# Performance work log

Measured on AMD Instinct MI355X. Metric: run time of the kernel, lower is better.

## Reference

```python
import jax, jax.numpy as jnp
import numpy as np

B, T, D, U = 128, 2048, 256, 512
ALPHA = 0.001


def hard_sigmoid(x):
    return jnp.clip(0.2 * x + 0.5, 0.0, 1.0)


def setup_inputs() -> dict:
    key = jax.random.key(0)
    k1, k2, k3 = jax.random.split(key, 3)
    x = jax.random.normal(k1, (B, T, D), dtype=jnp.float32)
    h0 = jnp.zeros((B, U), dtype=jnp.float32)
    c0 = jnp.zeros((B, U), dtype=jnp.float32)
    t0 = jnp.zeros((B, U), dtype=jnp.float32)
    # glorot-ish kernels
    kernel = jax.random.normal(k2, (D, 4 * U), dtype=jnp.float32) * (1.0 / np.sqrt(D))
    recurrent_kernel = jax.random.normal(k3, (U, 4 * U), dtype=jnp.float32) * (1.0 / np.sqrt(U))
    # bias zeros with forget-gate slice = 1 (unit_forget_bias)
    bias = jnp.zeros((4 * U,), dtype=jnp.float32).at[U:2 * U].set(1.0)
    # timegate: rows = period ~ U(10,100), shift ~ U(0,1000), r_on = 0.05
    rng = np.random.RandomState(0)
    timegate_kernel = jnp.asarray(
        np.vstack((rng.uniform(10, 100, U), rng.uniform(0, 1000, U), np.zeros(U) + 0.05)),
        dtype=jnp.float32)
    return {"x": x, "h0": h0, "c0": c0, "t0": t0, "kernel": kernel,
            "recurrent_kernel": recurrent_kernel, "bias": bias,
            "timegate_kernel": timegate_kernel}


def reference(x, h0, c0, t0, kernel, recurrent_kernel, bias, timegate_kernel):
    period = timegate_kernel[0]  # [U]
    shift = timegate_kernel[1]   # [U]
    r_on = timegate_kernel[2]    # [U]

    def step(carry, x_t):
        h, c, t = carry
        t = t + 1.0
        # fused gate pre-activations: [B, 4U]
        z = x_t @ kernel + h @ recurrent_kernel + bias
        zi, zf, zc, zo = jnp.split(z, 4, axis=-1)
        i = hard_sigmoid(zi)
        f = hard_sigmoid(zf)
        c_hat = f * c + i * jnp.tanh(zc)
        o = hard_sigmoid(zo)
        h_hat = o * jnp.tanh(c_hat)
        # phased time gate
        phi = (t - shift - period * jnp.floor((t - shift) / period)) / period
        k = jnp.where(phi <= r_on * 0.5, 2.0 * phi / r_on,
                      jnp.where(phi <= r_on, 2.0 - 2.0 * phi / r_on, ALPHA * phi))
        c_new = k * c_hat + (1.0 - k) * c
        h_new = k * h_hat + (1.0 - k) * h
        return (h_new, c_new, t), h_new

    xs = jnp.swapaxes(x, 0, 1)  # [T, B, D]
    (_, _, _), hs = jax.lax.scan(step, (h0, c0, t0), xs)
    return jnp.swapaxes(hs, 0, 1)  # [B, T, U]
```

## Files before the change

### kernel.cpp

```cpp
#include <hip/hip_runtime.h>
#include <hip/hip_bf16.h>
#include <math.h>

#define B_ 128
#define T_ 2048
#define D_ 256
#define U_ 512
#define G4_ 2048
#define KT_ 768
#define ALPHA_ 0.001f

#define NGROUP 8
#define GB 16
#define NSLICE 32
#define SU 16
#define NWG (NGROUP*NSLICE)
#define NTH 256
#define BU (B_*U_)

typedef __attribute__((ext_vector_type(8))) short bf16x8;
typedef __attribute__((ext_vector_type(4))) float f32x4;
typedef __attribute__((ext_vector_type(4))) int i32x4;
typedef __attribute__((ext_vector_type(2))) int i32x2;
typedef __attribute__((ext_vector_type(4))) unsigned short us4;

#define OFF_WT 0
#define OFF_H32 (G4_*KT_*2)
#define OFF_CNT (OFF_H32 + 2*BU*4)
#define CNT_DW (NGROUP*64)

__device__ __forceinline__ unsigned short f2b(float f) {
  unsigned u = __builtin_bit_cast(unsigned, f);
  u += 0x7fffu + ((u >> 16) & 1u);
  return (unsigned short)(u >> 16);
}

__device__ __forceinline__ float ftanh(float v) {
  v = fminf(fmaxf(v, -15.f), 15.f);
  float e = __expf(2.f * v);
  return (e - 1.f) * __builtin_amdgcn_rcpf(e + 1.f);
}

__global__ void prep_kernel(const float* __restrict__ kern,
                            const float* __restrict__ rker,
                            const float* __restrict__ h0,
                            unsigned short* __restrict__ wt,
                            unsigned* __restrict__ h32,
                            unsigned* __restrict__ cnt) {
  int idx = blockIdx.x * blockDim.x + threadIdx.x;
  int stride = gridDim.x * blockDim.x;
  for (int i = idx; i < G4_ * KT_; i += stride) {
    int col = i / KT_, k = i - col * KT_;
    float v = (k < U_) ? rker[(size_t)k * G4_ + col]
                       : kern[(size_t)(k - U_) * G4_ + col];
    wt[i] = f2b(v);
  }
  for (int i = idx; i < BU; i += stride) {
    h32[i] = ((unsigned)f2b(h0[i]) << 16);
    h32[BU + i] = 0xFFFFu;
  }
  for (int i = idx; i < CNT_DW; i += stride) cnt[i] = 0u;
}

#define LOAD8()                                                        \
  asm volatile(                                                        \
      "global_load_dwordx4 %0, %8, off sc0 sc1\n\t"                    \
      "global_load_dwordx4 %1, %8, off offset:1024 sc0 sc1\n\t"        \
      "global_load_dwordx4 %2, %8, off offset:2048 sc0 sc1\n\t"        \
      "global_load_dwordx4 %3, %8, off offset:3072 sc0 sc1\n\t"        \
      "global_load_dwordx4 %4, %9, off sc0 sc1\n\t"                    \
      "global_load_dwordx4 %5, %9, off offset:1024 sc0 sc1\n\t"        \
      "global_load_dwordx4 %6, %9, off offset:2048 sc0 sc1\n\t"        \
      "global_load_dwordx4 %7, %9, off offset:3072 sc0 sc1"            \
      : "=&v"(v0), "=&v"(v1), "=&v"(v2), "=&v"(v3),                    \
        "=&v"(v4), "=&v"(v5), "=&v"(v6), "=&v"(v7)                     \
      : "v"(ppoll), "v"(ppoll2));                                      \
  __builtin_amdgcn_sched_barrier(0)

#define FENCE8()                                                       \
  asm volatile("s_waitcnt vmcnt(0)"                                    \
      : "+v"(v0), "+v"(v1), "+v"(v2), "+v"(v3),                        \
        "+v"(v4), "+v"(v5), "+v"(v6), "+v"(v7));                       \
  __builtin_amdgcn_sched_barrier(0)

#define CKV(vv) ((((unsigned)(vv)[0] ^ tgv) & 0xffffu) |               \
                 (((unsigned)(vv)[1] ^ tgv) & 0xffffu) |               \
                 (((unsigned)(vv)[2] ^ tgv) & 0xffffu) |               \
                 (((unsigned)(vv)[3] ^ tgv) & 0xffffu))

#define PK(lo, hi) (int)(((unsigned)(hi) & 0xffff0000u) | ((unsigned)(lo) >> 16))

#define PACK2(vv, k)                                                         \
  { const int r_ = 4 * wv + ((k) >> 1);                                      \
    const int ba_ = (r_ * 1024 + (((k) & 1) << 9) + 8 * ln) ^ ((r_ & 7) << 4); \
    i32x2 d_ = { PK((vv)[0], (vv)[1]), PK((vv)[2], (vv)[3]) };               \
    *(i32x2*)(hdst + ba_) = d_; }

__global__ __launch_bounds__(NTH, 1) void plstm_kernel(
    const float* __restrict__ x, const float* __restrict__ h0,
    const float* __restrict__ c0, const float* __restrict__ t0,
    const float* __restrict__ bias, const float* __restrict__ tg,
    const unsigned short* __restrict__ wt,
    unsigned* h32, unsigned* cnt, float* __restrict__ out) {
  const int wg = blockIdx.x;
  const int g = wg & 7, sl = wg >> 3;
  const int b0 = g * GB, u0 = sl * SU;
  const int tid = threadIdx.x;
  const int wave = tid >> 6, lane = tid & 63;

  __shared__ unsigned short h_lds[2][GB * U_];
  __shared__ unsigned short x_lds[2][GB * D_];
  __shared__ float z_lds[2][GB][68];
  __shared__ unsigned wgarr[4];

  bf16x8 br[16], bx[8];
  {
    const int kr0 = (lane >> 4) * 8;
    const int col0 = wave * U_ + u0 + (lane & 15);
    const unsigned short* w0 = wt + (size_t)col0 * KT_;
#pragma unroll
    for (int kt = 0; kt < 16; ++kt) br[kt] = *(const bf16x8*)(w0 + kt * 32 + kr0);
#pragma unroll
    for (int kt = 0; kt < 8; ++kt)  bx[kt] = *(const bf16x8*)(w0 + U_ + kt * 32 + kr0);
  }
  const float bias_l = bias[wave * U_ + u0 + (lane & 15)];

  const int srow = tid >> 4;
  const int j = tid & 15;
  const int bb = b0 + srow;
  const int uu = u0 + j;
  float c_st = c0[bb * U_ + uu];
  float h_st = h0[bb * U_ + uu];
  const float t_0 = t0[bb * U_ + uu];
  const float per = tg[uu];
  const float shf = tg[U_ + uu];
  const float ron = tg[2 * U_ + uu];

  const int arow = lane & 15;
  const int koff = (lane >> 4) * 16;
  const int swzA = (arow & 7) << 4;
  const int swzR = (srow & 7) << 4;
  const int wv = wave, ln = lane;

  auto stage_x = [&](int t, int buf) {
    const int f0 = j * 16;
    const float* xp = x + ((size_t)bb * T_ + t) * D_ + f0;
    char* base = (char*)&x_lds[buf][0];
#pragma unroll
    for (int q = 0; q < 4; ++q) {
      float4 v = *(const float4*)(xp + q * 4);
      us4 pk = { f2b(v.x), f2b(v.y), f2b(v.z), f2b(v.w) };
      *(us4*)(base + ((srow * 512 + (f0 + q * 4) * 2) ^ swzR)) = pk;
    }
  };

  stage_x(0, 0);
  stage_x(1, 1);
  if (tid < 4) wgarr[tid] = 0u;
  __syncthreads();

  const unsigned* gslab0 = h32 + (size_t)b0 * U_;
  const int poff = wave * 2048 + lane * 4;
  unsigned* cnt_g = cnt + g * 64;

  for (int step = 0; step < T_; ++step) {
    const int par = step & 1;

    if (step > 0) {
      const unsigned tgt = 32u * (unsigned)step;
      while (__hip_atomic_load(cnt_g, __ATOMIC_RELAXED,
                               __HIP_MEMORY_SCOPE_AGENT) < tgt)
        __builtin_amdgcn_s_sleep(1);
    }

    const unsigned* ppoll = gslab0 + (size_t)par * BU + poff;
    const unsigned* ppoll2 = ppoll + 1024;
    i32x4 v0, v1, v2, v3, v4, v5, v6, v7;
    LOAD8();

    float kk;
    {
      float xx = t_0 + (float)(step + 1) - shf;
      float ph = (xx - per * floorf(xx / per)) / per;
      kk = (ph <= 0.5f * ron) ? (2.f * ph / ron)
         : ((ph <= ron) ? (2.f - 2.f * ph / ron) : (ALPHA_ * ph));
    }
    f32x4 aa = { bias_l, bias_l, bias_l, bias_l };
    f32x4 ab = { 0.f, 0.f, 0.f, 0.f };
    {
      const char* xb = (const char*)&x_lds[par][0];
#pragma unroll
      for (int kt = 0; kt < 8; ++kt) {
        bf16x8 a = *(const bf16x8*)(xb + ((arow * 512 + kt * 64 + koff) ^ swzA));
        if (kt & 1) ab = __builtin_amdgcn_mfma_f32_16x16x32_bf16(a, bx[kt], ab, 0, 0, 0);
        else        aa = __builtin_amdgcn_mfma_f32_16x16x32_bf16(a, bx[kt], aa, 0, 0, 0);
      }
    }

    const unsigned tgv = (unsigned)step;
    FENCE8();
    for (;;) {
      unsigned bad = CKV(v0) | CKV(v1) | CKV(v2) | CKV(v3) |
                     CKV(v4) | CKV(v5) | CKV(v6) | CKV(v7);
      if (!bad) break;
      __builtin_amdgcn_s_sleep(1);
      LOAD8();
      FENCE8();
    }

    {
      char* hdst = (char*)&h_lds[par][0];
      PACK2(v0, 0); PACK2(v1, 1); PACK2(v2, 2); PACK2(v3, 3);
      PACK2(v4, 4); PACK2(v5, 5); PACK2(v6, 6); PACK2(v7, 7);
    }
    __syncthreads();

    {
      const char* hbm = (const char*)&h_lds[par][0];
#pragma unroll
      for (int kt = 0; kt < 16; ++kt) {
        bf16x8 a = *(const bf16x8*)(hbm + ((arow * 1024 + kt * 64 + koff) ^ swzA));
        if (kt & 1) ab = __builtin_amdgcn_mfma_f32_16x16x32_bf16(a, br[kt], ab, 0, 0, 0);
        else        aa = __builtin_amdgcn_mfma_f32_16x16x32_bf16(a, br[kt], aa, 0, 0, 0);
      }
    }
    const f32x4 acc = aa + ab;

#pragma unroll
    for (int r2 = 0; r2 < 4; ++r2)
      z_lds[par][(lane >> 4) * 4 + r2][wave * 16 + (lane & 15)] = acc[r2];
    __syncthreads();

    float chat;
    {
      const float* zr = &z_lds[par][srow][0];
      const float zi = zr[j], zf = zr[16 + j], zc = zr[32 + j], zo = zr[48 + j];
      float ig = fminf(fmaxf(0.2f * zi + 0.5f, 0.f), 1.f);
      float fg = fminf(fmaxf(0.2f * zf + 0.5f, 0.f), 1.f);
      float og = fminf(fmaxf(0.2f * zo + 0.5f, 0.f), 1.f);
      chat = fg * c_st + ig * ftanh(zc);
      float hhat = og * ftanh(chat);
      h_st = kk * hhat + (1.f - kk) * h_st;
      unsigned hv = ((unsigned)f2b(h_st) << 16) | (unsigned)(step + 1);
      const unsigned* hp = h32 + (size_t)((step + 1) & 1) * BU + bb * U_ + uu;
      asm volatile("global_store_dword %0, %1, off sc0 sc1"
                   :: "v"(hp), "v"(hv) : "memory");
    }

    if (lane == 0) {
      unsigned old = atomicAdd(&wgarr[step & 3], 1u);
      if (old == 3u) {
        wgarr[step & 3] = 0u;
        atomicAdd(cnt_g, 1u);
      }
    }

    c_st = kk * chat + (1.f - kk) * c_st;
    out[((size_t)bb * T_ + step) * U_ + uu] = h_st;
    if (step + 2 < T_) stage_x(step + 2, par);
  }
}

extern "C" void kernel_launch(void* const* d_in, const int* in_sizes, int n_in,
                              void* d_out, int out_size, void* d_ws,
                              size_t ws_size, hipStream_t stream) {
  const float* x    = (const float*)d_in[0];
  const float* h0   = (const float*)d_in[1];
  const float* c0   = (const float*)d_in[2];
  const float* t0   = (const float*)d_in[3];
  const float* kern = (const float*)d_in[4];
  const float* rker = (const float*)d_in[5];
  const float* bias = (const float*)d_in[6];
  const float* tg   = (const float*)d_in[7];
  float* out = (float*)d_out;

  char* ws = (char*)d_ws;
  unsigned short* wt = (unsigned short*)(ws + OFF_WT);
  unsigned* h32      = (unsigned*)(ws + OFF_H32);
  unsigned* cnt      = (unsigned*)(ws + OFF_CNT);

  prep_kernel<<<1024, 256, 0, stream>>>(kern, rker, h0, wt, h32, cnt);
  plstm_kernel<<<NWG, NTH, 0, stream>>>(x, h0, c0, t0, bias, tg, wt, h32,
                                        cnt, out);
}
```

Baseline: 5.210 ms.

## Replace counter barrier with tagged-data polling and move x staging earlier

Removes the per-group global atomic counter and the LDS workgroup aggregation. Each step now waits by polling a few tagged h words, with double-buffered loads, until the step tag appears. It then relies on the existing tag checks over the full slab. Staging of the next x tile moves to just after the h pack barrier, so it overlaps with the MFMA work. This is meant to cut the atomic round trip and serialization on the critical path of the recurrence. In exchange, every wave spins on global memory, and the sampled polls only approximate full readiness, which the full check still covers.

```diff
diff --git a/kernel.cpp b/kernel.cpp
--- a/kernel.cpp
+++ b/kernel.cpp
@@ -26,8 +26,6 @@
 
 #define OFF_WT 0
 #define OFF_H32 (G4_*KT_*2)
-#define OFF_CNT (OFF_H32 + 2*BU*4)
-#define CNT_DW (NGROUP*64)
 
 __device__ __forceinline__ unsigned short f2b(float f) {
   unsigned u = __builtin_bit_cast(unsigned, f);
@@ -45,8 +43,7 @@
                             const float* __restrict__ rker,
                             const float* __restrict__ h0,
                             unsigned short* __restrict__ wt,
-                            unsigned* __restrict__ h32,
-                            unsigned* __restrict__ cnt) {
+                            unsigned* __restrict__ h32) {
   int idx = blockIdx.x * blockDim.x + threadIdx.x;
   int stride = gridDim.x * blockDim.x;
   for (int i = idx; i < G4_ * KT_; i += stride) {
@@ -59,7 +56,6 @@
     h32[i] = ((unsigned)f2b(h0[i]) << 16);
     h32[BU + i] = 0xFFFFu;
   }
-  for (int i = idx; i < CNT_DW; i += stride) cnt[i] = 0u;
 }
 
 #define LOAD8()                                                        \
@@ -80,7 +76,20 @@
 #define FENCE8()                                                       \
   asm volatile("s_waitcnt vmcnt(0)"                                    \
       : "+v"(v0), "+v"(v1), "+v"(v2), "+v"(v3),                        \
-        "+v"(v4), "+v"(v5), "+v"(v6), "+v"(v7));                       \
+        "+v"(v4), "+v"(v5), "+v"(v6), "+v"(v7),                        \
+        "+v"(dA0), "+v"(dA1), "+v"(dB0), "+v"(dB1));                   \
+  __builtin_amdgcn_sched_barrier(0)
+
+#define POLL2(a, b)                                                    \
+  asm volatile(                                                        \
+      "global_load_dword %0, %2, off sc0 sc1\n\t"                      \
+      "global_load_dword %1, %3, off sc0 sc1"                          \
+      : "=&v"(a), "=&v"(b) : "v"(s0p), "v"(s1p));                      \
+  __builtin_amdgcn_sched_barrier(0)
+
+#define WAITP()                                                        \
+  asm volatile("s_waitcnt vmcnt(2)"                                    \
+      : "+v"(dA0), "+v"(dA1), "+v"(dB0), "+v"(dB1));                   \
   __builtin_amdgcn_sched_barrier(0)
 
 #define CKV(vv) ((((unsigned)(vv)[0] ^ tgv) & 0xffffu) |               \
@@ -101,7 +110,7 @@
     const float* __restrict__ c0, const float* __restrict__ t0,
     const float* __restrict__ bias, const float* __restrict__ tg,
     const unsigned short* __restrict__ wt,
-    unsigned* h32, unsigned* cnt, float* __restrict__ out) {
+    unsigned* h32, float* __restrict__ out) {
   const int wg = blockIdx.x;
   const int g = wg & 7, sl = wg >> 3;
   const int b0 = g * GB, u0 = sl * SU;
@@ -111,7 +120,6 @@
   __shared__ unsigned short h_lds[2][GB * U_];
   __shared__ unsigned short x_lds[2][GB * D_];
   __shared__ float z_lds[2][GB][68];
-  __shared__ unsigned wgarr[4];
 
   bf16x8 br[16], bx[8];
   {
@@ -156,25 +164,35 @@
 
   stage_x(0, 0);
   stage_x(1, 1);
-  if (tid < 4) wgarr[tid] = 0u;
   __syncthreads();
 
   const unsigned* gslab0 = h32 + (size_t)b0 * U_;
   const int poff = wave * 2048 + lane * 4;
-  unsigned* cnt_g = cnt + g * 64;
+
+  unsigned dA0 = 0, dA1 = 0, dB0 = 0, dB1 = 0;
 
   for (int step = 0; step < T_; ++step) {
     const int par = step & 1;
-
-    if (step > 0) {
-      const unsigned tgt = 32u * (unsigned)step;
-      while (__hip_atomic_load(cnt_g, __ATOMIC_RELAXED,
-                               __HIP_MEMORY_SCOPE_AGENT) < tgt)
-        __builtin_amdgcn_s_sleep(1);
-    }
-
     const unsigned* ppoll = gslab0 + (size_t)par * BU + poff;
     const unsigned* ppoll2 = ppoll + 1024;
+
+    if (step > 0) {
+      asm volatile("s_waitcnt vmcnt(0)" ::: "memory");
+      const unsigned* s0p = ppoll;
+      const unsigned* s1p = ppoll + 256;
+      const unsigned tgp = (unsigned)step;
+      POLL2(dA0, dA1);
+      POLL2(dB0, dB1);
+      for (;;) {
+        WAITP();
+        if (__all((int)((((dA0 ^ tgp) | (dA1 ^ tgp)) & 0xffffu) == 0))) break;
+        POLL2(dA0, dA1);
+        WAITP();
+        if (__all((int)((((dB0 ^ tgp) | (dB1 ^ tgp)) & 0xffffu) == 0))) break;
+        POLL2(dB0, dB1);
+      }
+    }
+
     i32x4 v0, v1, v2, v3, v4, v5, v6, v7;
     LOAD8();
 
@@ -214,6 +232,8 @@
       PACK2(v4, 4); PACK2(v5, 5); PACK2(v6, 6); PACK2(v7, 7);
     }
     __syncthreads();
+
+    if (step + 2 < T_) stage_x(step + 2, par);
 
     {
       const char* hbm = (const char*)&h_lds[par][0];
@@ -247,17 +267,8 @@
                    :: "v"(hp), "v"(hv) : "memory");
     }
 
-    if (lane == 0) {
-      unsigned old = atomicAdd(&wgarr[step & 3], 1u);
-      if (old == 3u) {
-        wgarr[step & 3] = 0u;
-        atomicAdd(cnt_g, 1u);
-      }
-    }
-
     c_st = kk * chat + (1.f - kk) * c_st;
     out[((size_t)bb * T_ + step) * U_ + uu] = h_st;
-    if (step + 2 < T_) stage_x(step + 2, par);
   }
 }
 
@@ -277,9 +288,7 @@
   char* ws = (char*)d_ws;
   unsigned short* wt = (unsigned short*)(ws + OFF_WT);
   unsigned* h32      = (unsigned*)(ws + OFF_H32);
-  unsigned* cnt      = (unsigned*)(ws + OFF_CNT);
-
-  prep_kernel<<<1024, 256, 0, stream>>>(kern, rker, h0, wt, h32, cnt);
-  plstm_kernel<<<NWG, NTH, 0, stream>>>(x, h0, c0, t0, bias, tg, wt, h32,
-                                        cnt, out);
-}
+
+  prep_kernel<<<1024, 256, 0, stream>>>(kern, rker, h0, wt, h32);
+  plstm_kernel<<<NWG, NTH, 0, stream>>>(x, h0, c0, t0, bias, tg, wt, h32, out);
+}
```

Result: slower. 6.258 ms (+20.1%).
